# Performance work log

Hardware: AMD Instinct MI355X
Metric: run time of the kernel (lower is better)

## Reference

```python
import jax, jax.numpy as jnp
import numpy as np

NUM_COLUMNS = 16
INPUT_DIM = 1024
NUM_NEURONS = 256
SPARSITY = 0.05
B, S = 4, 2048


def setup_inputs() -> dict:
    key = jax.random.key(0)
    ks = jax.random.split(key, 12)
    D, C, N = INPUT_DIM, NUM_COLUMNS, NUM_NEURONS
    inp = {
        'x': jax.random.normal(ks[0], (B, S, D), dtype=jnp.float32),
        'col_emb': jax.random.normal(ks[1], (C, D), dtype=jnp.float32) * 0.02,
        'gate_w1': jax.random.normal(ks[2], (D, D // 2), dtype=jnp.float32) / np.sqrt(D),
        'gate_b1': jnp.zeros((D // 2,), dtype=jnp.float32),
        'gate_w2': jax.random.normal(ks[3], (D // 2, C), dtype=jnp.float32) / np.sqrt(D // 2),
        'gate_b2': jnp.zeros((C,), dtype=jnp.float32),
        'W_cols': jax.random.normal(ks[4], (C, D, N), dtype=jnp.float32) / np.sqrt(D),
        'b_cols': jnp.zeros((C, N), dtype=jnp.float32),
        'proj_w': jax.random.normal(ks[5], (C * N, D), dtype=jnp.float32) / np.sqrt(C * N),
        'proj_b': jnp.zeros((D,), dtype=jnp.float32),
        'ln_g': jnp.ones((D,), dtype=jnp.float32),
        'ln_b': jnp.zeros((D,), dtype=jnp.float32),
    }
    return inp


def _l2norm(v, axis=-1, eps=1e-12):
    n = jnp.sqrt(jnp.sum(v * v, axis=axis, keepdims=True))
    return v / jnp.maximum(n, eps)


def reference(x, col_emb, gate_w1, gate_b1, gate_w2, gate_b2, W_cols, b_cols,
              proj_w, proj_b, ln_g, ln_b):
    Bq, Sq, D = x.shape
    C = col_emb.shape[0]
    # --- router ---
    similarity = jnp.einsum('bsd,cd->bsc', _l2norm(x), _l2norm(col_emb))
    h = jax.nn.gelu(x @ gate_w1 + gate_b1, approximate=False)
    gate_values = jax.nn.sigmoid(h @ gate_w2 + gate_b2)
    logits = similarity + gate_values  # [B,S,C]
    k = max(1, int(C * SPARSITY))
    _, top_idx = jax.lax.top_k(logits, k)
    mask = jnp.sum(jax.nn.one_hot(top_idx, C, dtype=logits.dtype), axis=-2)  # [B,S,C]
    weights = mask * jax.nn.softmax(logits, axis=-1)
    # --- per-column compute (grouped GEMM), weighted combine ---
    cols = jax.nn.gelu(jnp.einsum('bsd,cdn->bscn', x, W_cols) + b_cols,
                       approximate=False)  # [B,S,C,N]
    cols = cols * weights[..., None]
    combined = cols.reshape(Bq, Sq, -1)  # [B,S,C*N], column-major concat order
    # --- proj + residual + layernorm ---
    y = combined @ proj_w + proj_b + x
    mu = jnp.mean(y, axis=-1, keepdims=True)
    var = jnp.mean((y - mu) ** 2, axis=-1, keepdims=True)
    out = (y - mu) * jax.lax.rsqrt(var + 1e-5) * ln_g + ln_b
    return out
```

## Files before the change

### kernel.cpp

```cpp
#include <hip/hip_runtime.h>
#include <hip/hip_bf16.h>
#include <math.h>

#define D    1024
#define C    16
#define N    256
#define TOK  8192
#define DH   512
#define RT_T 16
#define WLG  160
#define BCAP 20

using bf16x8 = __attribute__((ext_vector_type(8))) short;
using f32x4  = __attribute__((ext_vector_type(4))) float;

__device__ __forceinline__ float gelu_exact(float v) {
    return 0.5f * v * (1.0f + erff(v * 0.70710678118654752440f));
}
__device__ __forceinline__ float sigmoidf_(float z) {
    return 1.0f / (1.0f + expf(-z));
}
__device__ __forceinline__ short f2bf(float f) {
    unsigned u = __float_as_uint(f);
    unsigned r = u + 0x7FFF + ((u >> 16) & 1);
    return (short)(r >> 16);
}
__device__ __forceinline__ float bf2f(short s) {
    return __uint_as_float(((unsigned)(unsigned short)s) << 16);
}

__device__ __forceinline__ void gload16(const void* g, void* l) {
    __builtin_amdgcn_global_load_lds(
        (const __attribute__((address_space(1))) unsigned int*)g,
        (__attribute__((address_space(3))) unsigned int*)l, 16, 0, 0);
}

#define STAGE2(buf, kk) do {                                   \
    const int ko_ = (kk) * 128;                                \
    char* lA_ = (char*)AB[buf][0] + ldsWo;                     \
    char* lB_ = (char*)AB[buf][1] + ldsWo;                     \
    gload16(gA0 + ko_, lA_);                                   \
    gload16(gA1 + ko_, lA_ + 1024);                            \
    gload16(gB0 + ko_, lB_);                                   \
    gload16(gB1 + ko_, lB_ + 1024);                            \
} while (0)

__device__ __forceinline__ void tconv_body(const float* __restrict__ src0,
        short* __restrict__ dst0, int R, int Cc, int bx, int by, int bz,
        float (*tile)[65], int tid) {
    const size_t bofs = (size_t)bz * R * Cc;
    const float* src = src0 + bofs;
    short* dst = dst0 + bofs;
    const int cBase = bx * 64;
    const int rBase = by * 64;
    const int rr = tid >> 4;
    const int cq = (tid & 15) * 4;
    #pragma unroll
    for (int h = 0; h < 4; ++h) {
        const int r = h * 16 + rr;
        const float4 v = *(const float4*)&src[(size_t)(rBase + r) * Cc + cBase + cq];
        tile[r][cq + 0] = v.x; tile[r][cq + 1] = v.y;
        tile[r][cq + 2] = v.z; tile[r][cq + 3] = v.w;
    }
    __syncthreads();
    #pragma unroll
    for (int h = 0; h < 4; ++h) {
        const int cc = h * 16 + rr;
        short4 o;
        o.x = f2bf(tile[cq + 0][cc]);
        o.y = f2bf(tile[cq + 1][cc]);
        o.z = f2bf(tile[cq + 2][cc]);
        o.w = f2bf(tile[cq + 3][cc]);
        *(short4*)&dst[(size_t)(cBase + cc) * R + rBase + cq] = o;
    }
}

__global__ __launch_bounds__(256) void prep_all_kernel(
        const float* __restrict__ x, const float* __restrict__ col_emb,
        const float* __restrict__ gate_w1, const float* __restrict__ W_cols,
        const float* __restrict__ proj_w,
        short* __restrict__ xb, short* __restrict__ w1T,
        short* __restrict__ WcT, short* __restrict__ pwT,
        float* __restrict__ cnorm) {
    __shared__ float tile[64][65];
    const int b = blockIdx.x;
    const int tid = threadIdx.x;
    if (b == 0) {
        const int c = tid >> 4, l = tid & 15;
        float acc = 0.f;
        for (int j = 0; j < 64; ++j) {
            float v = col_emb[c * D + l + 16 * j];
            acc += v * v;
        }
        for (int off = 8; off; off >>= 1) acc += __shfl_xor(acc, off, 16);
        if (l == 0) cnorm[c] = fmaxf(sqrtf(acc), 1e-12f);
    } else if (b < 2049) {
        const int base = (b - 1) * 1024;
        #pragma unroll
        for (int h = 0; h < 4; ++h) {
            const int i = base + h * 256 + tid;
            const float4 v = ((const float4*)x)[i];
            short4 o;
            o.x = f2bf(v.x); o.y = f2bf(v.y); o.z = f2bf(v.z); o.w = f2bf(v.w);
            ((short4*)xb)[i] = o;
        }
    } else if (b < 2177) {
        const int idx = b - 2049;
        tconv_body(gate_w1, w1T, D, DH, idx & 7, idx >> 3, 0, tile, tid);
    } else if (b < 3201) {
        const int idx = b - 2177;
        tconv_body(W_cols, WcT, D, N, idx & 3, (idx >> 2) & 15, idx >> 6, tile, tid);
    } else {
        const int idx = b - 3201;
        tconv_body(proj_w, pwT, N, D, idx & 15, (idx >> 4) & 3, idx >> 6, tile, tid);
    }
}

__global__ __launch_bounds__(256) void gate_mfma_kernel(
        const short* __restrict__ Ag, const short* __restrict__ BTg,
        const float* __restrict__ bias, short* __restrict__ outb) {
    __shared__ short AB[2][2][64 * 64];
    const int tid = threadIdx.x;
    const int lane = tid & 63;
    const int wave = tid >> 6;
    const int wr = wave >> 1, wc = wave & 1;

    const size_t m0 = (size_t)blockIdx.x * 64;
    const int n0 = blockIdx.y * 64;

    const int r0 = wave * 16 + (lane >> 3);
    const int r1 = r0 + 8;
    const int bl = (lane & 7) * 16;
    const int b0 = bl ^ ((r0 & 7) << 4);
    const int b1 = bl ^ ((r1 & 7) << 4);
    const char* gA0 = (const char*)Ag + (m0 + r0) * (size_t)(D * 2) + b0;
    const char* gA1 = (const char*)Ag + (m0 + r1) * (size_t)(D * 2) + b1;
    const char* gB0 = (const char*)BTg + (size_t)(n0 + r0) * (D * 2) + b0;
    const char* gB1 = (const char*)BTg + (size_t)(n0 + r1) * (D * 2) + b1;
    const int ldsWo = wave * 2048;

    const int mrow = wr * 32 + (lane & 15);
    const int nrow = wc * 32 + (lane & 15);
    const int kb0 = (lane >> 4) * 16;
    const int swm = (mrow & 7) << 4;
    const int swn = (nrow & 7) << 4;

    f32x4 acc[2][2] = {};
    STAGE2(0, 0);
    __syncthreads();
    for (int kk = 0; kk < D / 64; ++kk) {
        const int cur = kk & 1;
        if (kk + 1 < D / 64) STAGE2(cur ^ 1, kk + 1);
        const char* As = (const char*)AB[cur][0];
        const char* Bs = (const char*)AB[cur][1];
        #pragma unroll
        for (int ks = 0; ks < 2; ++ks) {
            const int kb = kb0 + ks * 64;
            bf16x8 aF[2], bF[2];
            #pragma unroll
            for (int i = 0; i < 2; ++i)
                aF[i] = *(const bf16x8*)(As + (mrow + i * 16) * 128 + (kb ^ swm));
            #pragma unroll
            for (int j = 0; j < 2; ++j)
                bF[j] = *(const bf16x8*)(Bs + (nrow + j * 16) * 128 + (kb ^ swn));
            #pragma unroll
            for (int i = 0; i < 2; ++i)
                #pragma unroll
                for (int j = 0; j < 2; ++j)
                    acc[i][j] = __builtin_amdgcn_mfma_f32_16x16x32_bf16(
                                    aF[i], bF[j], acc[i][j], 0, 0, 0);
        }
        __syncthreads();
    }
    const int crow = (lane >> 4) * 4;
    const int ccol = lane & 15;
    #pragma unroll
    for (int i = 0; i < 2; ++i)
        #pragma unroll
        for (int j = 0; j < 2; ++j) {
            const int n = n0 + wc * 32 + j * 16 + ccol;
            const float bb = bias[n];
            #pragma unroll
            for (int r = 0; r < 4; ++r) {
                const int m = (int)m0 + wr * 32 + i * 16 + crow + r;
                outb[(size_t)m * DH + n] = f2bf(gelu_exact(acc[i][j][r] + bb));
            }
        }
}

template<int MODE>
__global__ __launch_bounds__(256) void mfma_tile(
        const short* __restrict__ Ag, const short* __restrict__ BTg,
        const float* __restrict__ bias, const float* __restrict__ x,
        const int* __restrict__ order, const float* __restrict__ wgt,
        const int* __restrict__ wl,
        short* __restrict__ outb, float* __restrict__ outf) {
    constexpr int KDIM = (MODE == 2) ? N : D;
    constexpr int KSTEPS = KDIM / 64;
    __shared__ short AB[2][2][64 * 64];
    __shared__ int   tokl[64];
    __shared__ float wgl[64];

    const int e = wl[blockIdx.x];
    if (e < 0) return;
    const int col  = e >> 24;
    const int nt   = (e >> 16) & 0xFF;
    const int base = e & 0xFFFF;

    const int tid = threadIdx.x;
    const int lane = tid & 63;
    const int wave = tid >> 6;
    const int wr = wave >> 1, wc = wave & 1;
    const int n0 = blockIdx.y * 64;

    if (tid < 64) {
        const int i = tid < nt ? tid : nt - 1;
        const int t = order[base + i];
        tokl[tid] = t;
        if (MODE == 1) wgl[tid] = wgt[t];
    }
    __syncthreads();

    const int r0 = wave * 16 + (lane >> 3);
    const int r1 = r0 + 8;
    const int bl = (lane & 7) * 16;
    const int b0 = bl ^ ((r0 & 7) << 4);
    const int b1 = bl ^ ((r1 & 7) << 4);
    const char* gA0; const char* gA1;
    if (MODE == 1) {
        gA0 = (const char*)Ag + (size_t)tokl[r0] * (D * 2) + b0;
        gA1 = (const char*)Ag + (size_t)tokl[r1] * (D * 2) + b1;
    } else {
        const int s0 = base + min(r0, nt - 1);
        const int s1 = base + min(r1, nt - 1);
        gA0 = (const char*)Ag + (size_t)s0 * (N * 2) + b0;
        gA1 = (const char*)Ag + (size_t)s1 * (N * 2) + b1;
    }
    const size_t bRowB = KDIM * 2;
    size_t bbase;
    if (MODE == 1) bbase = ((size_t)col * N + n0) * bRowB;
    else           bbase = ((size_t)col * D + n0) * bRowB;
    const char* gB0 = (const char*)BTg + bbase + (size_t)r0 * bRowB + b0;
    const char* gB1 = (const char*)BTg + bbase + (size_t)r1 * bRowB + b1;
    const int ldsWo = wave * 2048;

    const int mrow = wr * 32 + (lane & 15);
    const int nrow = wc * 32 + (lane & 15);
    const int kb0 = (lane >> 4) * 16;
    const int swm = (mrow & 7) << 4;
    const int swn = (nrow & 7) << 4;

    f32x4 acc[2][2] = {};
    STAGE2(0, 0);
    __syncthreads();
    for (int kk = 0; kk < KSTEPS; ++kk) {
        const int cur = kk & 1;
        if (kk + 1 < KSTEPS) STAGE2(cur ^ 1, kk + 1);
        const char* As = (const char*)AB[cur][0];
        const char* Bs = (const char*)AB[cur][1];
        #pragma unroll
        for (int ks = 0; ks < 2; ++ks) {
            const int kb = kb0 + ks * 64;
            bf16x8 aF[2], bF[2];
            #pragma unroll
            for (int i = 0; i < 2; ++i)
                aF[i] = *(const bf16x8*)(As + (mrow + i * 16) * 128 + (kb ^ swm));
            #pragma unroll
            for (int j = 0; j < 2; ++j)
                bF[j] = *(const bf16x8*)(Bs + (nrow + j * 16) * 128 + (kb ^ swn));
            #pragma unroll
            for (int i = 0; i < 2; ++i)
                #pragma unroll
                for (int j = 0; j < 2; ++j)
                    acc[i][j] = __builtin_amdgcn_mfma_f32_16x16x32_bf16(
                                    aF[i], bF[j], acc[i][j], 0, 0, 0);
        }
        __syncthreads();
    }

    const int crow = (lane >> 4) * 4;
    const int ccol = lane & 15;
    if (MODE == 1) {
        #pragma unroll
        for (int i = 0; i < 2; ++i)
            #pragma unroll
            for (int j = 0; j < 2; ++j) {
                const int n = n0 + wc * 32 + j * 16 + ccol;
                const float bb = bias[col * N + n];
                #pragma unroll
                for (int r = 0; r < 4; ++r) {
                    const int il = wr * 32 + i * 16 + crow + r;
                    if (il < nt) {
                        const float v = gelu_exact(acc[i][j][r] + bb) * wgl[il];
                        outb[(size_t)(base + il) * N + n] = f2bf(v);
                    }
                }
            }
    } else {
        #pragma unroll
        for (int i = 0; i < 2; ++i)
            #pragma unroll
            for (int j = 0; j < 2; ++j) {
                const int dcol = n0 + wc * 32 + j * 16 + ccol;
                const float bb = bias[dcol];
                #pragma unroll
                for (int r = 0; r < 4; ++r) {
                    const int il = wr * 32 + i * 16 + crow + r;
                    if (il < nt) {
                        const size_t ofs = (size_t)tokl[il] * D + dcol;
                        outf[ofs] = acc[i][j][r] + bb + x[ofs];
                    }
                }
            }
    }
}

__global__ __launch_bounds__(256) void route_kernel(
        const float* __restrict__ x, const short* __restrict__ Hb,
        const float* __restrict__ col_emb, const float* __restrict__ cnorm,
        const float* __restrict__ w2, const float* __restrict__ b2,
        int* __restrict__ idx, float* __restrict__ wgt) {
    __shared__ float P[256][33];
    __shared__ float Q[8][33];
    __shared__ float SSW[4];
    __shared__ float FL[RT_T][34];
    const int tid = threadIdx.x;
    const int lane = tid & 63;
    const int t0 = blockIdx.x * RT_T;
    const int swz = (tid & 7) << 2;

    float4 ce[C];
    #pragma unroll
    for (int c = 0; c < C; ++c)
        ce[c] = *(const float4*)&col_emb[c * D + tid * 4];
    float w2r[2][C];
    #pragma unroll
    for (int r2 = 0; r2 < 2; ++r2)
        #pragma unroll
        for (int cq = 0; cq < 4; ++cq) {
            const float4 v = *(const float4*)&w2[(tid * 2 + r2) * C + cq * 4];
            w2r[r2][cq * 4 + 0] = v.x; w2r[r2][cq * 4 + 1] = v.y;
            w2r[r2][cq * 4 + 2] = v.z; w2r[r2][cq * 4 + 3] = v.w;
        }

    for (int ti = 0; ti < RT_T; ++ti) {
        const int t = t0 + ti;
        const float4 xv = *(const float4*)&x[(size_t)t * D + tid * 4];
        const unsigned hu = *(const unsigned*)&Hb[(size_t)t * DH + tid * 2];
        const float h0 = bf2f((short)(hu & 0xffff));
        const float h1 = bf2f((short)(hu >> 16));
        float pv[32];
        #pragma unroll
        for (int c = 0; c < C; ++c)
            pv[c] = xv.x * ce[c].x + xv.y * ce[c].y + xv.z * ce[c].z + xv.w * ce[c].w;
        #pragma unroll
        for (int c = 0; c < C; ++c)
            pv[C + c] = h0 * w2r[0][c] + h1 * w2r[1][c];
        float ssp = xv.x * xv.x + xv.y * xv.y + xv.z * xv.z + xv.w * xv.w;
        #pragma unroll
        for (int off = 32; off; off >>= 1) ssp += __shfl_xor(ssp, off);
        if (lane == 0) SSW[tid >> 6] = ssp;
        #pragma unroll
        for (int c = 0; c < 32; ++c)
            P[tid][c ^ swz] = pv[c];
        __syncthreads();
        {
            const int v = tid & 31, jj = tid >> 5;
            float s = 0.f;
            #pragma unroll
            for (int k = 0; k < 32; ++k) {
                const int row = jj * 32 + k;
                s += P[row][v ^ ((row & 7) << 2)];
            }
            Q[jj][v] = s;
        }
        __syncthreads();
        if (tid < 32) {
            float f = 0.f;
            #pragma unroll
            for (int j2 = 0; j2 < 8; ++j2) f += Q[j2][tid];
            FL[ti][tid] = f;
        } else if (tid == 32) {
            FL[ti][32] = SSW[0] + SSW[1] + SSW[2] + SSW[3];
        }
        __syncthreads();
    }

    if (tid < RT_T) {
        const int t = t0 + tid;
        const float xn = fmaxf(sqrtf(FL[tid][32]), 1e-12f);
        float logit[C];
        #pragma unroll
        for (int c = 0; c < C; ++c)
            logit[c] = FL[tid][c] / (xn * cnorm[c])
                     + sigmoidf_(FL[tid][C + c] + b2[c]);
        float mx = logit[0]; int am = 0;
        #pragma unroll
        for (int c = 1; c < C; ++c)
            if (logit[c] > mx) { mx = logit[c]; am = c; }
        float se = 0.f;
        #pragma unroll
        for (int c = 0; c < C; ++c) se += expf(logit[c] - mx);
        idx[t] = am;
        wgt[t] = 1.f / se;
    }
}

__global__ __launch_bounds__(256) void hist_kernel(const int* __restrict__ idx,
        int* __restrict__ cursor, int* __restrict__ wl) {
    __shared__ int h[C];
    const int tid = threadIdx.x;
    if (tid < C) h[tid] = 0;
    for (int i = tid; i < WLG; i += 256) wl[i] = -1;
    __syncthreads();
    for (int t = tid; t < TOK; t += 256) atomicAdd(&h[idx[t]], 1);
    __syncthreads();
    if (tid == 0) {
        int s = 0;
        int slots[8] = {0, 0, 0, 0, 0, 0, 0, 0};
        for (int c = 0; c < C; ++c) {
            cursor[c] = s;
            for (int st = 0; st < h[c]; st += 64) {
                const int ntg = min(64, h[c] - st);
                int b = c & 7;
                while (slots[b] >= BCAP) b = (b + 1) & 7;
                wl[slots[b] * 8 + b] = (c << 24) | (ntg << 16) | (s + st);
                slots[b]++;
            }
            s += h[c];
        }
    }
}

__global__ __launch_bounds__(256) void scatter_kernel(const int* __restrict__ idx,
        int* __restrict__ cursor, int* __restrict__ order) {
    __shared__ int lh[C];
    __shared__ int lbase[C];
    const int tid = threadIdx.x;
    const int t = blockIdx.x * 256 + tid;
    if (tid < C) lh[tid] = 0;
    __syncthreads();
    const int c = idx[t];
    const int p = atomicAdd(&lh[c], 1);
    __syncthreads();
    if (tid < C) lbase[tid] = atomicAdd(&cursor[tid], lh[tid]);
    __syncthreads();
    order[lbase[c] + p] = t;
}

__global__ __launch_bounds__(256) void ln_kernel(float* __restrict__ out,
        const float* __restrict__ g, const float* __restrict__ b) {
    __shared__ float wr_[4], wr2[4];
    const int t = blockIdx.x, tid = threadIdx.x;
    const float4 v = *(const float4*)&out[(size_t)t * D + tid * 4];
    float s = v.x + v.y + v.z + v.w;
    float s2 = v.x * v.x + v.y * v.y + v.z * v.z + v.w * v.w;
    for (int off = 32; off; off >>= 1) { s += __shfl_xor(s, off); s2 += __shfl_xor(s2, off); }
    if ((tid & 63) == 0) { wr_[tid >> 6] = s; wr2[tid >> 6] = s2; }
    __syncthreads();
    const float sum = wr_[0] + wr_[1] + wr_[2] + wr_[3];
    const float sum2 = wr2[0] + wr2[1] + wr2[2] + wr2[3];
    const float mu = sum * (1.f / D);
    const float var = sum2 * (1.f / D) - mu * mu;
    const float inv = rsqrtf(var + 1e-5f);
    const float4 g4 = *(const float4*)&g[tid * 4];
    const float4 b4 = *(const float4*)&b[tid * 4];
    float4 o;
    o.x = (v.x - mu) * inv * g4.x + b4.x;
    o.y = (v.y - mu) * inv * g4.y + b4.y;
    o.z = (v.z - mu) * inv * g4.z + b4.z;
    o.w = (v.w - mu) * inv * g4.w + b4.w;
    *(float4*)&out[(size_t)t * D + tid * 4] = o;
}

extern "C" void kernel_launch(void* const* d_in, const int* in_sizes, int n_in,
                              void* d_out, int out_size, void* d_ws, size_t ws_size,
                              hipStream_t stream) {
    const float* x       = (const float*)d_in[0];
    const float* col_emb = (const float*)d_in[1];
    const float* gate_w1 = (const float*)d_in[2];
    const float* gate_b1 = (const float*)d_in[3];
    const float* gate_w2 = (const float*)d_in[4];
    const float* gate_b2 = (const float*)d_in[5];
    const float* W_cols  = (const float*)d_in[6];
    const float* b_cols  = (const float*)d_in[7];
    const float* proj_w  = (const float*)d_in[8];
    const float* proj_b  = (const float*)d_in[9];
    const float* ln_g    = (const float*)d_in[10];
    const float* ln_b    = (const float*)d_in[11];
    float* out = (float*)d_out;

    char* w = (char*)d_ws;
    short* xb    = (short*)w;  w += (size_t)TOK * D * 2;
    short* Hb    = (short*)w;  w += (size_t)TOK * DH * 2;
    short* actb  = (short*)w;  w += (size_t)TOK * N * 2 + 65536;
    short* w1T   = (short*)w;  w += (size_t)DH * D * 2;
    short* WcT   = (short*)w;  w += (size_t)C * N * D * 2;
    short* pwT   = (short*)w;  w += (size_t)C * D * N * 2;
    float* wgt   = (float*)w;  w += TOK * 4;
    float* cnorm = (float*)w;  w += 64;
    int*   idx   = (int*)w;    w += TOK * 4;
    int*   order = (int*)w;    w += TOK * 4;
    int*   cursor= (int*)w;    w += 64;
    int*   wl    = (int*)w;    w += WLG * 4;

    hipLaunchKernelGGL(prep_all_kernel, dim3(4225), dim3(256), 0, stream,
                       x, col_emb, gate_w1, W_cols, proj_w,
                       xb, w1T, WcT, pwT, cnorm);
    hipLaunchKernelGGL(gate_mfma_kernel, dim3(TOK / 64, DH / 64), dim3(256), 0, stream,
                       xb, w1T, gate_b1, Hb);
    hipLaunchKernelGGL(route_kernel, dim3(TOK / RT_T), dim3(256), 0, stream,
                       x, Hb, col_emb, cnorm, gate_w2, gate_b2, idx, wgt);
    hipLaunchKernelGGL(hist_kernel, dim3(1), dim3(256), 0, stream, idx, cursor, wl);
    hipLaunchKernelGGL(scatter_kernel, dim3(TOK / 256), dim3(256), 0, stream,
                       idx, cursor, order);
    hipLaunchKernelGGL((mfma_tile<1>), dim3(WLG, N / 64), dim3(256), 0, stream,
                       xb, WcT, b_cols, nullptr, order, wgt, wl, actb, nullptr);
    hipLaunchKernelGGL((mfma_tile<2>), dim3(WLG, D / 64), dim3(256), 0, stream,
                       actb, pwT, proj_b, x, order, wgt, wl, nullptr, out);
    hipLaunchKernelGGL(ln_kernel, dim3(TOK), dim3(256), 0, stream, out, ln_g, ln_b);
}
```

Measured before the change: 156.9 us.

## Enlarge gate GEMM tile, hold proj A-operand in registers, use ballot histogram

The gate GEMM moves from 64x64 to 128x64 tiles, so each wave computes a 64x32 sub-tile and the B tile is reused across more rows. The proj GEMM now loads its whole 64x256 activation A-tile straight into registers up front and stages only B through LDS, which removes the A LDS round-trip. The templated column kernel becomes a dedicated col1_kernel, and the histogram replaces per-token LDS atomics with wave ballots and popcounts. In exchange, register pressure rises and the gate grid has half as many blocks.

```diff
diff --git a/kernel.cpp b/kernel.cpp
--- a/kernel.cpp
+++ b/kernel.cpp
@@ -34,16 +34,6 @@
         (const __attribute__((address_space(1))) unsigned int*)g,
         (__attribute__((address_space(3))) unsigned int*)l, 16, 0, 0);
 }
-
-#define STAGE2(buf, kk) do {                                   \
-    const int ko_ = (kk) * 128;                                \
-    char* lA_ = (char*)AB[buf][0] + ldsWo;                     \
-    char* lB_ = (char*)AB[buf][1] + ldsWo;                     \
-    gload16(gA0 + ko_, lA_);                                   \
-    gload16(gA1 + ko_, lA_ + 1024);                            \
-    gload16(gB0 + ko_, lB_);                                   \
-    gload16(gB1 + ko_, lB_ + 1024);                            \
-} while (0)
 
 __device__ __forceinline__ void tconv_body(const float* __restrict__ src0,
         short* __restrict__ dst0, int R, int Cc, int bx, int by, int bz,
@@ -119,24 +109,132 @@
 __global__ __launch_bounds__(256) void gate_mfma_kernel(
         const short* __restrict__ Ag, const short* __restrict__ BTg,
         const float* __restrict__ bias, short* __restrict__ outb) {
-    __shared__ short AB[2][2][64 * 64];
+    __shared__ short AB[2][(128 + 64) * 64];
     const int tid = threadIdx.x;
     const int lane = tid & 63;
     const int wave = tid >> 6;
     const int wr = wave >> 1, wc = wave & 1;
 
-    const size_t m0 = (size_t)blockIdx.x * 64;
+    const size_t m0 = (size_t)blockIdx.x * 128;
     const int n0 = blockIdx.y * 64;
+
+    const int rl = lane >> 3;
+    const int bl = (lane & 7) * 16;
+    const char* gAh[4];
+    #pragma unroll
+    for (int h = 0; h < 4; ++h) {
+        const int r = wave * 32 + h * 8 + rl;
+        gAh[h] = (const char*)Ag + (m0 + r) * (size_t)(D * 2) + (bl ^ ((r & 7) << 4));
+    }
+    const char* gBh[2];
+    #pragma unroll
+    for (int h = 0; h < 2; ++h) {
+        const int r = wave * 16 + h * 8 + rl;
+        gBh[h] = (const char*)BTg + (size_t)(n0 + r) * (D * 2) + (bl ^ ((r & 7) << 4));
+    }
+
+    const int swz = ((lane & 7)) << 4;
+    const int kb0 = (lane >> 4) * 16;
+
+    f32x4 acc[4][2] = {};
+    {
+        char* Ab = (char*)AB[0];
+        char* Bb = (char*)AB[0] + 16384;
+        #pragma unroll
+        for (int h = 0; h < 4; ++h) gload16(gAh[h], Ab + (wave * 32 + h * 8) * 128);
+        #pragma unroll
+        for (int h = 0; h < 2; ++h) gload16(gBh[h], Bb + (wave * 16 + h * 8) * 128);
+    }
+    __syncthreads();
+    for (int kk = 0; kk < D / 64; ++kk) {
+        const int cur = kk & 1;
+        if (kk + 1 < D / 64) {
+            const int ko = (kk + 1) * 128;
+            char* Ab = (char*)AB[cur ^ 1];
+            char* Bb = (char*)AB[cur ^ 1] + 16384;
+            #pragma unroll
+            for (int h = 0; h < 4; ++h) gload16(gAh[h] + ko, Ab + (wave * 32 + h * 8) * 128);
+            #pragma unroll
+            for (int h = 0; h < 2; ++h) gload16(gBh[h] + ko, Bb + (wave * 16 + h * 8) * 128);
+        }
+        const char* As = (const char*)AB[cur];
+        const char* Bs = As + 16384;
+        #pragma unroll
+        for (int ks = 0; ks < 2; ++ks) {
+            const int kb = kb0 + ks * 64;
+            bf16x8 aF[4], bF[2];
+            #pragma unroll
+            for (int i = 0; i < 4; ++i)
+                aF[i] = *(const bf16x8*)(As + (wr * 64 + i * 16 + (lane & 15)) * 128
+                                         + (kb ^ swz));
+            #pragma unroll
+            for (int j = 0; j < 2; ++j)
+                bF[j] = *(const bf16x8*)(Bs + (wc * 32 + j * 16 + (lane & 15)) * 128
+                                         + (kb ^ swz));
+            #pragma unroll
+            for (int i = 0; i < 4; ++i)
+                #pragma unroll
+                for (int j = 0; j < 2; ++j)
+                    acc[i][j] = __builtin_amdgcn_mfma_f32_16x16x32_bf16(
+                                    aF[i], bF[j], acc[i][j], 0, 0, 0);
+        }
+        __syncthreads();
+    }
+    const int crow = (lane >> 4) * 4;
+    const int ccol = lane & 15;
+    #pragma unroll
+    for (int i = 0; i < 4; ++i)
+        #pragma unroll
+        for (int j = 0; j < 2; ++j) {
+            const int n = n0 + wc * 32 + j * 16 + ccol;
+            const float bb = bias[n];
+            #pragma unroll
+            for (int r = 0; r < 4; ++r) {
+                const int m = (int)m0 + wr * 64 + i * 16 + crow + r;
+                outb[(size_t)m * DH + n] = f2bf(gelu_exact(acc[i][j][r] + bb));
+            }
+        }
+}
+
+__global__ __launch_bounds__(256) void col1_kernel(
+        const short* __restrict__ Ag, const short* __restrict__ BTg,
+        const float* __restrict__ bias,
+        const int* __restrict__ order, const float* __restrict__ wgt,
+        const int* __restrict__ wl, short* __restrict__ outb) {
+    __shared__ short AB[2][2][64 * 64];
+    __shared__ int   tokl[64];
+    __shared__ float wgl[64];
+
+    const int e = wl[blockIdx.x];
+    if (e < 0) return;
+    const int col  = e >> 24;
+    const int nt   = (e >> 16) & 0xFF;
+    const int base = e & 0xFFFF;
+
+    const int tid = threadIdx.x;
+    const int lane = tid & 63;
+    const int wave = tid >> 6;
+    const int wr = wave >> 1, wc = wave & 1;
+    const int n0 = blockIdx.y * 64;
+
+    if (tid < 64) {
+        const int i = tid < nt ? tid : nt - 1;
+        const int t = order[base + i];
+        tokl[tid] = t;
+        wgl[tid] = wgt[t];
+    }
+    __syncthreads();
 
     const int r0 = wave * 16 + (lane >> 3);
     const int r1 = r0 + 8;
     const int bl = (lane & 7) * 16;
     const int b0 = bl ^ ((r0 & 7) << 4);
     const int b1 = bl ^ ((r1 & 7) << 4);
-    const char* gA0 = (const char*)Ag + (m0 + r0) * (size_t)(D * 2) + b0;
-    const char* gA1 = (const char*)Ag + (m0 + r1) * (size_t)(D * 2) + b1;
-    const char* gB0 = (const char*)BTg + (size_t)(n0 + r0) * (D * 2) + b0;
-    const char* gB1 = (const char*)BTg + (size_t)(n0 + r1) * (D * 2) + b1;
+    const char* gA0 = (const char*)Ag + (size_t)tokl[r0] * (D * 2) + b0;
+    const char* gA1 = (const char*)Ag + (size_t)tokl[r1] * (D * 2) + b1;
+    const size_t bbase = ((size_t)col * N + n0) * (D * 2);
+    const char* gB0 = (const char*)BTg + bbase + (size_t)r0 * (D * 2) + b0;
+    const char* gB1 = (const char*)BTg + bbase + (size_t)r1 * (D * 2) + b1;
     const int ldsWo = wave * 2048;
 
     const int mrow = wr * 32 + (lane & 15);
@@ -146,11 +244,22 @@
     const int swn = (nrow & 7) << 4;
 
     f32x4 acc[2][2] = {};
-    STAGE2(0, 0);
+    {
+        char* lA = (char*)AB[0][0] + ldsWo;
+        char* lB = (char*)AB[0][1] + ldsWo;
+        gload16(gA0, lA); gload16(gA1, lA + 1024);
+        gload16(gB0, lB); gload16(gB1, lB + 1024);
+    }
     __syncthreads();
     for (int kk = 0; kk < D / 64; ++kk) {
         const int cur = kk & 1;
-        if (kk + 1 < D / 64) STAGE2(cur ^ 1, kk + 1);
+        if (kk + 1 < D / 64) {
+            const int ko = (kk + 1) * 128;
+            char* lA = (char*)AB[cur ^ 1][0] + ldsWo;
+            char* lB = (char*)AB[cur ^ 1][1] + ldsWo;
+            gload16(gA0 + ko, lA); gload16(gA1 + ko, lA + 1024);
+            gload16(gB0 + ko, lB); gload16(gB1 + ko, lB + 1024);
+        }
         const char* As = (const char*)AB[cur][0];
         const char* Bs = (const char*)AB[cur][1];
         #pragma unroll
@@ -172,6 +281,7 @@
         }
         __syncthreads();
     }
+
     const int crow = (lane >> 4) * 4;
     const int ccol = lane & 15;
     #pragma unroll
@@ -179,27 +289,25 @@
         #pragma unroll
         for (int j = 0; j < 2; ++j) {
             const int n = n0 + wc * 32 + j * 16 + ccol;
-            const float bb = bias[n];
+            const float bb = bias[col * N + n];
             #pragma unroll
             for (int r = 0; r < 4; ++r) {
-                const int m = (int)m0 + wr * 32 + i * 16 + crow + r;
-                outb[(size_t)m * DH + n] = f2bf(gelu_exact(acc[i][j][r] + bb));
+                const int il = wr * 32 + i * 16 + crow + r;
+                if (il < nt) {
+                    const float v = gelu_exact(acc[i][j][r] + bb) * wgl[il];
+                    outb[(size_t)(base + il) * N + n] = f2bf(v);
+                }
             }
         }
 }
 
-template<int MODE>
-__global__ __launch_bounds__(256) void mfma_tile(
+__global__ __launch_bounds__(256) void proj_kernel(
         const short* __restrict__ Ag, const short* __restrict__ BTg,
         const float* __restrict__ bias, const float* __restrict__ x,
-        const int* __restrict__ order, const float* __restrict__ wgt,
-        const int* __restrict__ wl,
-        short* __restrict__ outb, float* __restrict__ outf) {
-    constexpr int KDIM = (MODE == 2) ? N : D;
-    constexpr int KSTEPS = KDIM / 64;
-    __shared__ short AB[2][2][64 * 64];
+        const int* __restrict__ order, const int* __restrict__ wl,
+        float* __restrict__ outf) {
+    __shared__ short Bs2[2][64 * 64];
     __shared__ int   tokl[64];
-    __shared__ float wgl[64];
 
     const int e = wl[blockIdx.x];
     if (e < 0) return;
@@ -213,58 +321,57 @@
     const int wr = wave >> 1, wc = wave & 1;
     const int n0 = blockIdx.y * 64;
 
+    bf16x8 aF[4][2][2];
+    #pragma unroll
+    for (int i = 0; i < 2; ++i) {
+        const int m = wr * 32 + i * 16 + (lane & 15);
+        const int s = base + min(m, nt - 1);
+        const char* ga = (const char*)Ag + (size_t)s * (N * 2) + (lane >> 4) * 16;
+        #pragma unroll
+        for (int kk = 0; kk < 4; ++kk)
+            #pragma unroll
+            for (int ks = 0; ks < 2; ++ks)
+                aF[kk][i][ks] = *(const bf16x8*)(ga + kk * 128 + ks * 64);
+    }
+
     if (tid < 64) {
         const int i = tid < nt ? tid : nt - 1;
-        const int t = order[base + i];
-        tokl[tid] = t;
-        if (MODE == 1) wgl[tid] = wgt[t];
-    }
-    __syncthreads();
+        tokl[tid] = order[base + i];
+    }
 
     const int r0 = wave * 16 + (lane >> 3);
     const int r1 = r0 + 8;
     const int bl = (lane & 7) * 16;
     const int b0 = bl ^ ((r0 & 7) << 4);
     const int b1 = bl ^ ((r1 & 7) << 4);
-    const char* gA0; const char* gA1;
-    if (MODE == 1) {
-        gA0 = (const char*)Ag + (size_t)tokl[r0] * (D * 2) + b0;
-        gA1 = (const char*)Ag + (size_t)tokl[r1] * (D * 2) + b1;
-    } else {
-        const int s0 = base + min(r0, nt - 1);
-        const int s1 = base + min(r1, nt - 1);
-        gA0 = (const char*)Ag + (size_t)s0 * (N * 2) + b0;
-        gA1 = (const char*)Ag + (size_t)s1 * (N * 2) + b1;
-    }
-    const size_t bRowB = KDIM * 2;
-    size_t bbase;
-    if (MODE == 1) bbase = ((size_t)col * N + n0) * bRowB;
-    else           bbase = ((size_t)col * D + n0) * bRowB;
-    const char* gB0 = (const char*)BTg + bbase + (size_t)r0 * bRowB + b0;
-    const char* gB1 = (const char*)BTg + bbase + (size_t)r1 * bRowB + b1;
+    const size_t bbase = ((size_t)col * D + n0) * (N * 2);
+    const char* gB0 = (const char*)BTg + bbase + (size_t)r0 * (N * 2) + b0;
+    const char* gB1 = (const char*)BTg + bbase + (size_t)r1 * (N * 2) + b1;
     const int ldsWo = wave * 2048;
 
-    const int mrow = wr * 32 + (lane & 15);
     const int nrow = wc * 32 + (lane & 15);
     const int kb0 = (lane >> 4) * 16;
-    const int swm = (mrow & 7) << 4;
     const int swn = (nrow & 7) << 4;
 
     f32x4 acc[2][2] = {};
-    STAGE2(0, 0);
-    __syncthreads();
-    for (int kk = 0; kk < KSTEPS; ++kk) {
+    {
+        char* lB = (char*)Bs2[0] + ldsWo;
+        gload16(gB0, lB); gload16(gB1, lB + 1024);
+    }
+    __syncthreads();
+    #pragma unroll
+    for (int kk = 0; kk < 4; ++kk) {
         const int cur = kk & 1;
-        if (kk + 1 < KSTEPS) STAGE2(cur ^ 1, kk + 1);
-        const char* As = (const char*)AB[cur][0];
-        const char* Bs = (const char*)AB[cur][1];
+        if (kk + 1 < 4) {
+            const int ko = (kk + 1) * 128;
+            char* lB = (char*)Bs2[cur ^ 1] + ldsWo;
+            gload16(gB0 + ko, lB); gload16(gB1 + ko, lB + 1024);
+        }
+        const char* Bs = (const char*)Bs2[cur];
         #pragma unroll
         for (int ks = 0; ks < 2; ++ks) {
             const int kb = kb0 + ks * 64;
-            bf16x8 aF[2], bF[2];
-            #pragma unroll
-            for (int i = 0; i < 2; ++i)
-                aF[i] = *(const bf16x8*)(As + (mrow + i * 16) * 128 + (kb ^ swm));
+            bf16x8 bF[2];
             #pragma unroll
             for (int j = 0; j < 2; ++j)
                 bF[j] = *(const bf16x8*)(Bs + (nrow + j * 16) * 128 + (kb ^ swn));
@@ -273,46 +380,28 @@
                 #pragma unroll
                 for (int j = 0; j < 2; ++j)
                     acc[i][j] = __builtin_amdgcn_mfma_f32_16x16x32_bf16(
-                                    aF[i], bF[j], acc[i][j], 0, 0, 0);
+                                    aF[kk][i][ks], bF[j], acc[i][j], 0, 0, 0);
         }
         __syncthreads();
     }
 
     const int crow = (lane >> 4) * 4;
     const int ccol = lane & 15;
-    if (MODE == 1) {
-        #pragma unroll
-        for (int i = 0; i < 2; ++i)
-            #pragma unroll
-            for (int j = 0; j < 2; ++j) {
-                const int n = n0 + wc * 32 + j * 16 + ccol;
-                const float bb = bias[col * N + n];
-                #pragma unroll
-                for (int r = 0; r < 4; ++r) {
-                    const int il = wr * 32 + i * 16 + crow + r;
-                    if (il < nt) {
-                        const float v = gelu_exact(acc[i][j][r] + bb) * wgl[il];
-                        outb[(size_t)(base + il) * N + n] = f2bf(v);
-                    }
+    #pragma unroll
+    for (int i = 0; i < 2; ++i)
+        #pragma unroll
+        for (int j = 0; j < 2; ++j) {
+            const int dcol = n0 + wc * 32 + j * 16 + ccol;
+            const float bb = bias[dcol];
+            #pragma unroll
+            for (int r = 0; r < 4; ++r) {
+                const int il = wr * 32 + i * 16 + crow + r;
+                if (il < nt) {
+                    const size_t ofs = (size_t)tokl[il] * D + dcol;
+                    outf[ofs] = acc[i][j][r] + bb + x[ofs];
                 }
             }
-    } else {
-        #pragma unroll
-        for (int i = 0; i < 2; ++i)
-            #pragma unroll
-            for (int j = 0; j < 2; ++j) {
-                const int dcol = n0 + wc * 32 + j * 16 + ccol;
-                const float bb = bias[dcol];
-                #pragma unroll
-                for (int r = 0; r < 4; ++r) {
-                    const int il = wr * 32 + i * 16 + crow + r;
-                    if (il < nt) {
-                        const size_t ofs = (size_t)tokl[il] * D + dcol;
-                        outf[ofs] = acc[i][j][r] + bb + x[ofs];
-                    }
-                }
-            }
-    }
+        }
 }
 
 __global__ __launch_bounds__(256) void route_kernel(
@@ -410,10 +499,21 @@
         int* __restrict__ cursor, int* __restrict__ wl) {
     __shared__ int h[C];
     const int tid = threadIdx.x;
+    const int lane = tid & 63;
+    const int wave = tid >> 6;
     if (tid < C) h[tid] = 0;
     for (int i = tid; i < WLG; i += 256) wl[i] = -1;
     __syncthreads();
-    for (int t = tid; t < TOK; t += 256) atomicAdd(&h[idx[t]], 1);
+    int cnt = 0;
+    for (int t0 = wave * 64; t0 < TOK; t0 += 256) {
+        const int c = idx[t0 + lane];
+        #pragma unroll
+        for (int cc = 0; cc < C; ++cc) {
+            const unsigned long long m = __ballot(c == cc);
+            if (lane == cc) cnt += (int)__popcll(m);
+        }
+    }
+    if (lane < C) atomicAdd(&h[lane], cnt);
     __syncthreads();
     if (tid == 0) {
         int s = 0;
@@ -507,16 +607,16 @@
     hipLaunchKernelGGL(prep_all_kernel, dim3(4225), dim3(256), 0, stream,
                        x, col_emb, gate_w1, W_cols, proj_w,
                        xb, w1T, WcT, pwT, cnorm);
-    hipLaunchKernelGGL(gate_mfma_kernel, dim3(TOK / 64, DH / 64), dim3(256), 0, stream,
+    hipLaunchKernelGGL(gate_mfma_kernel, dim3(TOK / 128, DH / 64), dim3(256), 0, stream,
                        xb, w1T, gate_b1, Hb);
     hipLaunchKernelGGL(route_kernel, dim3(TOK / RT_T), dim3(256), 0, stream,
                        x, Hb, col_emb, cnorm, gate_w2, gate_b2, idx, wgt);
     hipLaunchKernelGGL(hist_kernel, dim3(1), dim3(256), 0, stream, idx, cursor, wl);
     hipLaunchKernelGGL(scatter_kernel, dim3(TOK / 256), dim3(256), 0, stream,
                        idx, cursor, order);
-    hipLaunchKernelGGL((mfma_tile<1>), dim3(WLG, N / 64), dim3(256), 0, stream,
-                       xb, WcT, b_cols, nullptr, order, wgt, wl, actb, nullptr);
-    hipLaunchKernelGGL((mfma_tile<2>), dim3(WLG, D / 64), dim3(256), 0, stream,
-                       actb, pwT, proj_b, x, order, wgt, wl, nullptr, out);
+    hipLaunchKernelGGL(col1_kernel, dim3(WLG, N / 64), dim3(256), 0, stream,
+                       xb, WcT, b_cols, order, wgt, wl, actb);
+    hipLaunchKernelGGL(proj_kernel, dim3(WLG, D / 64), dim3(256), 0, stream,
+                       actb, pwT, proj_b, x, order, wl, out);
     hipLaunchKernelGGL(ln_kernel, dim3(TOK), dim3(256), 0, stream, out, ln_g, ln_b);
 }
```

New measurement: 177.4 us. +13.0%, slower.
